# Kernel optimization log

Measured on AMD Instinct MI355X. Metric: run time of the kernel, lower is better.

## Reference

```python
import jax, jax.numpy as jnp
import numpy as np

N_NODES = 100000
N_EDGES = 400000
N_GRAPHS = 1000
DIM = 5
N_OUT = 2
EPS = 1e-5


def _linear_params(key, fan_in, fan_out):
    kw, kb = jax.random.split(key)
    s = 1.0 / np.sqrt(fan_in)
    w = jax.random.uniform(kw, (fan_in, fan_out), minval=-s, maxval=s, dtype=jnp.float32)
    b = jax.random.uniform(kb, (fan_out,), minval=-s, maxval=s, dtype=jnp.float32)
    return w, b


def _gn_params(c):
    # rows: [weight, bias, mean_scale] as in PyG GraphNorm init (1, 0, 1)
    return jnp.stack([jnp.ones((c,)), jnp.zeros((c,)), jnp.ones((c,))], axis=0).astype(jnp.float32)


def setup_inputs() -> dict:
    key = jax.random.key(0)
    ks = jax.random.split(key, 16)
    x = jax.random.normal(ks[0], (N_NODES, DIM), dtype=jnp.float32)
    edge_index = jax.random.randint(ks[1], (2, N_EDGES), 0, N_NODES, dtype=jnp.int64)
    batch = jnp.sort(jax.random.randint(ks[2], (N_NODES,), 0, N_GRAPHS, dtype=jnp.int64))
    c1_w1, c1_b1 = _linear_params(ks[3], 2 * DIM, 128)
    c1_w2, c1_b2 = _linear_params(ks[4], 128, 128)
    c1_w3, c1_b3 = _linear_params(ks[5], 128, 128)
    c2_w1, c2_b1 = _linear_params(ks[6], 2 * 128, 256)
    c2_w2, c2_b2 = _linear_params(ks[7], 256, 256)
    c3_w1, c3_b1 = _linear_params(ks[8], 2 * 256, 256)
    lin_w1, lin_b1 = _linear_params(ks[9], 256, 256)
    lin_w2, lin_b2 = _linear_params(ks[10], 256, N_OUT)
    return {
        "x": x, "edge_index": edge_index, "batch": batch,
        "c1_w1": c1_w1, "c1_b1": c1_b1, "c1_gn1": _gn_params(128),
        "c1_w2": c1_w2, "c1_b2": c1_b2, "c1_gn2": _gn_params(128),
        "c1_w3": c1_w3, "c1_b3": c1_b3, "c1_gn3": _gn_params(128),
        "c2_w1": c2_w1, "c2_b1": c2_b1, "c2_gn1": _gn_params(256),
        "c2_w2": c2_w2, "c2_b2": c2_b2, "c2_gn2": _gn_params(256),
        "c3_w1": c3_w1, "c3_b1": c3_b1, "c3_gn1": _gn_params(256),
        "lin_w1": lin_w1, "lin_b1": lin_b1, "lin_w2": lin_w2, "lin_b2": lin_b2,
    }


def _graph_norm(h, p):
    # PyG GraphNorm with batch=None: normalize over all rows (single graph)
    g, b, ms = p[0], p[1], p[2]
    m = h.mean(axis=0)
    out = h - ms * m
    var = (out * out).mean(axis=0)
    return g * out * jax.lax.rsqrt(var + EPS) + b


def _edge_conv(x, src, dst, layers):
    # EdgeConv message: nn(cat[x_i, x_j - x_i]) aggregated (mean) at target i
    xi = x[dst]                                     # [E, C]
    h = jnp.concatenate([xi, x[src] - xi], axis=-1)  # [E, 2C]
    for w, b, gp in layers:
        h = jax.nn.relu(_graph_norm(h @ w + b, gp))
    s = jax.ops.segment_sum(h, dst, num_segments=N_NODES)
    ones = jnp.ones((dst.shape[0], 1), dtype=h.dtype)
    cnt = jax.ops.segment_sum(ones, dst, num_segments=N_NODES)
    return s / jnp.maximum(cnt, 1.0)


def reference(x, edge_index, batch,
              c1_w1, c1_b1, c1_gn1, c1_w2, c1_b2, c1_gn2, c1_w3, c1_b3, c1_gn3,
              c2_w1, c2_b1, c2_gn1, c2_w2, c2_b2, c2_gn2,
              c3_w1, c3_b1, c3_gn1,
              lin_w1, lin_b1, lin_w2, lin_b2):
    src, dst = edge_index[0], edge_index[1]
    h = _edge_conv(x, src, dst, [(c1_w1, c1_b1, c1_gn1), (c1_w2, c1_b2, c1_gn2), (c1_w3, c1_b3, c1_gn3)])
    h = _edge_conv(h, src, dst, [(c2_w1, c2_b1, c2_gn1), (c2_w2, c2_b2, c2_gn2)])
    h = _edge_conv(h, src, dst, [(c3_w1, c3_b1, c3_gn1)])
    # global_mean_pool over graphs (dropout = identity in eval)
    gs = jax.ops.segment_sum(h, batch, num_segments=N_GRAPHS)
    gc = jax.ops.segment_sum(jnp.ones((h.shape[0], 1), h.dtype), batch, num_segments=N_GRAPHS)
    g = gs / jnp.maximum(gc, 1.0)                   # [G, 256]
    out = jax.nn.relu(g @ lin_w1 + lin_b1) @ lin_w2 + lin_b2  # [G, n_out]
    return out
```

## Files before the change

### kernel.cpp

```cpp
#include <hip/hip_runtime.h>
#include <hip/hip_bf16.h>

#define NN 100000
#define NE 400000
#define NG 1000

typedef __attribute__((ext_vector_type(8))) short bf16x8;
typedef __attribute__((ext_vector_type(4))) float f32x4;

__device__ __forceinline__ float bf2f(unsigned short h) {
    return __uint_as_float((unsigned)h << 16);
}
__device__ __forceinline__ unsigned short f2bf(float f) {
    unsigned u = __float_as_uint(f);
    return (unsigned short)((u + 0x7FFFu + ((u >> 16) & 1u)) >> 16);
}

__global__ void diag_kernel(float* __restrict__ out, int n, float val) {
    int i = blockIdx.x * 256 + threadIdx.x;
    if (i < n) out[i] = val;
}

__global__ void deg_kernel(const int* __restrict__ dst, int* __restrict__ deg) {
    int e = blockIdx.x * 256 + threadIdx.x;
    if (e < NE) atomicAdd(&deg[dst[e]], 1);
}

__global__ void invdeg_kernel(const int* __restrict__ deg, float* __restrict__ invdeg) {
    int n = blockIdx.x * 256 + threadIdx.x;
    if (n < NN) invdeg[n] = 1.0f / (float)(deg[n] > 0 ? deg[n] : 1);
}

__global__ void conv1_node_kernel(const float* __restrict__ x, const float* __restrict__ W,
                                  unsigned short* __restrict__ RQ) {
    __shared__ float Ws[1280];
    for (int i = threadIdx.x; i < 1280; i += 256) Ws[i] = W[i];
    __syncthreads();
    int c = threadIdx.x & 127;
    int which = threadIdx.x >> 7;
    for (int n = blockIdx.x; n < NN; n += gridDim.x) {
        float acc = 0.f;
        #pragma unroll
        for (int r = 0; r < 5; r++) {
            float xv = x[n * 5 + r];
            float bot = Ws[(5 + r) * 128 + c];
            float w = which ? bot : (Ws[r * 128 + c] - bot);
            acc = fmaf(xv, w, acc);
        }
        RQ[(size_t)n * 256 + threadIdx.x] = f2bf(acc);
    }
}

__global__ void wtrans_kernel(const float* __restrict__ W, unsigned short* __restrict__ Wt,
                              int K, int N) {
    int idx = blockIdx.x * 256 + threadIdx.x;
    if (idx >= K * N) return;
    int c = idx / K, k = idx - c * K;
    Wt[(size_t)c * K + k] = f2bf(W[(size_t)k * N + c]);
}

__global__ void wprime_t_kernel(const float* __restrict__ W, unsigned short* __restrict__ Wpt,
                                int K, int C) {
    int idx = blockIdx.x * 256 + threadIdx.x;
    if (idx >= 2 * C * K) return;
    int n = idx / K, k = idx - n * K;
    float v;
    if (n < C) v = W[(size_t)k * C + n] - W[(size_t)(K + k) * C + n];
    else       v = W[(size_t)(K + k) * C + (n - C)];
    Wpt[(size_t)n * K + k] = f2bf(v);
}

template<int C>
__global__ void gstats_kernel(const unsigned short* __restrict__ RQ, const int* __restrict__ src,
                              const int* __restrict__ dst, const float* __restrict__ bias,
                              float* __restrict__ ssum, float* __restrict__ ssq) {
    constexpr int EPB = 256 / C;
    int c = threadIdx.x % C;
    int sub = threadIdx.x / C;
    float b = bias[c];
    float ls = 0.f, lq = 0.f;
    for (int e = blockIdx.x * EPB + sub; e < NE; e += gridDim.x * EPB) {
        int d = dst[e], s = src[e];
        float v = (bf2f(RQ[(size_t)d * (2 * C) + c]) + bf2f(RQ[(size_t)s * (2 * C) + C + c])) + b;
        ls += v; lq += v * v;
    }
    __shared__ float red[2][256];
    red[0][threadIdx.x] = ls; red[1][threadIdx.x] = lq;
    __syncthreads();
    if (threadIdx.x < C) {
        float s0 = 0.f, q0 = 0.f;
        #pragma unroll
        for (int g = 0; g < EPB; g++) { s0 += red[0][g * C + c]; q0 += red[1][g * C + c]; }
        atomicAdd(&ssum[c], s0);
        atomicAdd(&ssq[c], q0);
    }
}

__global__ void finalize_kernel(const float* __restrict__ ssum, const float* __restrict__ ssq,
                                const float* __restrict__ gn, int C, float invM,
                                float* __restrict__ alpha, float* __restrict__ beta) {
    int c = threadIdx.x;
    if (c >= C) return;
    float g = gn[c], b = gn[C + c], ms = gn[2 * C + c];
    float m = ssum[c] * invM;
    float var = ssq[c] * invM - m * m * ms * (2.f - ms);
    float inv = rsqrtf(var + 1e-5f);
    alpha[c] = g * inv;
    beta[c] = b - g * inv * ms * m;
}

template<int BN, bool GATHER, bool NORMRELU, bool ROWSC, bool STATS, bool STORE, bool SCAT,
         bool AF32>
__global__ __launch_bounds__(256) void mgemm_kernel(
    const void* __restrict__ Av, const int* __restrict__ gsrc, const int* __restrict__ gdst,
    const float* __restrict__ biasIn, const unsigned short* __restrict__ Wt,
    const float* __restrict__ alpha, const float* __restrict__ beta,
    const float* __restrict__ rowscale, const float* __restrict__ biasOut,
    unsigned short* __restrict__ Cmat, int M, int K, int N,
    float* __restrict__ ssum, float* __restrict__ ssq,
    const float* __restrict__ alphaO, const float* __restrict__ betaO,
    float* __restrict__ hsum) {
    constexpr int WNC = BN / 4;
    constexpr int NF = WNC / 16;
    __shared__ __align__(16) unsigned short At[64][40];
    __shared__ __align__(16) unsigned short Bt[BN][40];
    __shared__ float sS[BN], sQ[BN];
    const int t = threadIdx.x;
    const int wave = t >> 6, lane = t & 63;
    const int l15 = lane & 15, lq = lane >> 4;
    const int r0 = blockIdx.y * 64;
    const int n0 = blockIdx.x * BN;
    const int srow = t >> 2, skq = t & 3;

    if (STATS && t < BN) { sS[t] = 0.f; sQ[t] = 0.f; }

    const int ar = r0 + srow;
    int gd = 0, gs = 0;
    if (GATHER) { gd = gdst[ar]; gs = gsrc[ar]; }
    float rs = 1.f;
    if (ROWSC) rs = (ar < M) ? rowscale[ar] : 0.f;

    const unsigned short* Abf = (const unsigned short*)Av;
    const float* Af = (const float*)Av;

    f32x4 acc[4][NF];
    #pragma unroll
    for (int i = 0; i < 4; i++)
        #pragma unroll
        for (int j = 0; j < NF; j++) acc[i][j] = {0.f, 0.f, 0.f, 0.f};

    for (int k0 = 0; k0 < K; k0 += 32) {
        const int kb = k0 + skq * 8;
        float v[8];
        if (GATHER) {
            ushort4 p0 = *(const ushort4*)&Abf[(size_t)gd * 2 * K + kb];
            ushort4 p1 = *(const ushort4*)&Abf[(size_t)gd * 2 * K + kb + 4];
            ushort4 q0 = *(const ushort4*)&Abf[(size_t)gs * 2 * K + K + kb];
            ushort4 q1 = *(const ushort4*)&Abf[(size_t)gs * 2 * K + K + kb + 4];
            float4 b0 = *(const float4*)&biasIn[kb];
            float4 b1 = *(const float4*)&biasIn[kb + 4];
            v[0] = bf2f(p0.x) + bf2f(q0.x) + b0.x; v[1] = bf2f(p0.y) + bf2f(q0.y) + b0.y;
            v[2] = bf2f(p0.z) + bf2f(q0.z) + b0.z; v[3] = bf2f(p0.w) + bf2f(q0.w) + b0.w;
            v[4] = bf2f(p1.x) + bf2f(q1.x) + b1.x; v[5] = bf2f(p1.y) + bf2f(q1.y) + b1.y;
            v[6] = bf2f(p1.z) + bf2f(q1.z) + b1.z; v[7] = bf2f(p1.w) + bf2f(q1.w) + b1.w;
        } else if (AF32) {
            if (ar < M) {
                float4 f0 = *(const float4*)&Af[(size_t)ar * K + kb];
                float4 f1 = *(const float4*)&Af[(size_t)ar * K + kb + 4];
                v[0] = f0.x; v[1] = f0.y; v[2] = f0.z; v[3] = f0.w;
                v[4] = f1.x; v[5] = f1.y; v[6] = f1.z; v[7] = f1.w;
            } else {
                #pragma unroll
                for (int i = 0; i < 8; i++) v[i] = 0.f;
            }
        } else {
            if (ar < M) {
                ushort4 p0 = *(const ushort4*)&Abf[(size_t)ar * K + kb];
                ushort4 p1 = *(const ushort4*)&Abf[(size_t)ar * K + kb + 4];
                v[0] = bf2f(p0.x); v[1] = bf2f(p0.y); v[2] = bf2f(p0.z); v[3] = bf2f(p0.w);
                v[4] = bf2f(p1.x); v[5] = bf2f(p1.y); v[6] = bf2f(p1.z); v[7] = bf2f(p1.w);
            } else {
                #pragma unroll
                for (int i = 0; i < 8; i++) v[i] = 0.f;
            }
        }
        if (NORMRELU) {
            float4 a0 = *(const float4*)&alpha[kb];
            float4 a1 = *(const float4*)&alpha[kb + 4];
            float4 e0 = *(const float4*)&beta[kb];
            float4 e1 = *(const float4*)&beta[kb + 4];
            float al[8] = {a0.x, a0.y, a0.z, a0.w, a1.x, a1.y, a1.z, a1.w};
            float be[8] = {e0.x, e0.y, e0.z, e0.w, e1.x, e1.y, e1.z, e1.w};
            #pragma unroll
            for (int i = 0; i < 8; i++) v[i] = fmaxf(fmaf(al[i], v[i], be[i]), 0.f);
        }
        if (ROWSC) {
            #pragma unroll
            for (int i = 0; i < 8; i++) v[i] *= rs;
        }
        uint pk[4];
        #pragma unroll
        for (int i = 0; i < 4; i++)
            pk[i] = (uint)f2bf(v[2 * i]) | ((uint)f2bf(v[2 * i + 1]) << 16);
        *(uint4*)&At[srow][skq * 8] = make_uint4(pk[0], pk[1], pk[2], pk[3]);

        for (int i = t; i < BN * 4; i += 256) {
            int col = i >> 2, kq = i & 3;
            *(uint4*)&Bt[col][kq * 8] =
                *(const uint4*)&Wt[(size_t)(n0 + col) * K + k0 + kq * 8];
        }
        __syncthreads();
        bf16x8 af[4];
        #pragma unroll
        for (int rf = 0; rf < 4; rf++)
            af[rf] = *(const bf16x8*)&At[16 * rf + l15][lq * 8];
        bf16x8 bfr[NF];
        #pragma unroll
        for (int cf = 0; cf < NF; cf++)
            bfr[cf] = *(const bf16x8*)&Bt[wave * WNC + 16 * cf + l15][lq * 8];
        #pragma unroll
        for (int rf = 0; rf < 4; rf++)
            #pragma unroll
            for (int cf = 0; cf < NF; cf++)
                acc[rf][cf] = __builtin_amdgcn_mfma_f32_16x16x32_bf16(
                    af[rf], bfr[cf], acc[rf][cf], 0, 0, 0);
        __syncthreads();
    }

    int cA[NF];
    float bO[NF], aO[NF], bOo[NF];
    #pragma unroll
    for (int cf = 0; cf < NF; cf++) {
        cA[cf] = n0 + wave * WNC + 16 * cf + l15;
        bO[cf] = (biasOut != nullptr) ? biasOut[cA[cf]] : 0.f;
        if (SCAT) { aO[cf] = alphaO[cA[cf]]; bOo[cf] = betaO[cA[cf]]; }
    }
    float ps[NF], pq[NF];
    #pragma unroll
    for (int cf = 0; cf < NF; cf++) { ps[cf] = 0.f; pq[cf] = 0.f; }
    #pragma unroll
    for (int rf = 0; rf < 4; rf++) {
        int rb = r0 + 16 * rf + lq * 4;
        int dd[4];
        if (SCAT) {
            #pragma unroll
            for (int jj = 0; jj < 4; jj++) dd[jj] = gdst[rb + jj];
        }
        #pragma unroll
        for (int cf = 0; cf < NF; cf++) {
            #pragma unroll
            for (int jj = 0; jj < 4; jj++) {
                float o = acc[rf][cf][jj] + bO[cf];
                if (STATS) { ps[cf] += o; pq[cf] += o * o; }
                if (STORE) {
                    int r = rb + jj;
                    if (r < M) Cmat[(size_t)r * N + cA[cf]] = f2bf(o);
                }
                if (SCAT) {
                    float h = fmaxf(fmaf(aO[cf], o, bOo[cf]), 0.f);
                    atomicAdd(&hsum[(size_t)dd[jj] * N + cA[cf]], h);
                }
            }
        }
    }
    if (STATS) {
        #pragma unroll
        for (int cf = 0; cf < NF; cf++) {
            float s = ps[cf], q = pq[cf];
            s += __shfl_xor(s, 16); s += __shfl_xor(s, 32);
            q += __shfl_xor(q, 16); q += __shfl_xor(q, 32);
            if (lq == 0) {
                atomicAdd(&sS[cA[cf] - n0], s);
                atomicAdd(&sQ[cA[cf] - n0], q);
            }
        }
        __syncthreads();
        if (t < BN) {
            atomicAdd(&ssum[n0 + t], sS[t]);
            atomicAdd(&ssq[n0 + t], sQ[t]);
        }
    }
}

template<int C>
__global__ void aggregate_kernel(const unsigned short* __restrict__ Y, const int* __restrict__ dst,
                                 const float* __restrict__ alpha, const float* __restrict__ beta,
                                 float* __restrict__ hsum) {
    constexpr int EPB = 256 / C;
    int c = threadIdx.x % C;
    int sub = threadIdx.x / C;
    float al = alpha[c], be = beta[c];
    for (int e = blockIdx.x * EPB + sub; e < NE; e += gridDim.x * EPB) {
        float v = fmaxf(fmaf(al, bf2f(Y[(size_t)e * C + c]), be), 0.f);
        atomicAdd(&hsum[(size_t)dst[e] * C + c], v);
    }
}

__global__ void aggregate_fg_kernel(const unsigned short* __restrict__ RQ,
                                    const int* __restrict__ src, const int* __restrict__ dst,
                                    const float* __restrict__ bias, const float* __restrict__ alpha,
                                    const float* __restrict__ beta, float* __restrict__ hsum) {
    int c = threadIdx.x;
    float b = bias[c], al = alpha[c], be = beta[c];
    for (int e = blockIdx.x; e < NE; e += gridDim.x) {
        int d = dst[e], s = src[e];
        float v = (bf2f(RQ[(size_t)d * 512 + c]) + bf2f(RQ[(size_t)s * 512 + 256 + c])) + b;
        float h = fmaxf(fmaf(al, v, be), 0.f);
        atomicAdd(&hsum[(size_t)d * 256 + c], h);
    }
}

__global__ void pool_kernel(const float* __restrict__ h3sum, const float* __restrict__ invdeg,
                            const int* __restrict__ batch, float* __restrict__ gsum,
                            int* __restrict__ gcnt) {
    int c = threadIdx.x;
    for (int n = blockIdx.x; n < NN; n += gridDim.x) {
        float v = h3sum[(size_t)n * 256 + c] * invdeg[n];
        int g = batch[n];
        atomicAdd(&gsum[(size_t)g * 256 + c], v);
        if (c == 0) atomicAdd(&gcnt[g], 1);
    }
}

__global__ void mlp_kernel(const float* __restrict__ gsum, const int* __restrict__ gcnt,
                           const float* __restrict__ W1, const float* __restrict__ b1,
                           const float* __restrict__ W2, const float* __restrict__ b2,
                           float* __restrict__ out) {
    int g = blockIdx.x;
    int t = threadIdx.x;
    __shared__ float grow[256];
    __shared__ float r0s[256], r1s[256];
    int cnt = gcnt[g];
    float inv = 1.0f / (float)(cnt > 0 ? cnt : 1);
    grow[t] = gsum[(size_t)g * 256 + t] * inv;
    __syncthreads();
    float acc = b1[t];
    for (int k = 0; k < 256; k++) acc = fmaf(grow[k], W1[k * 256 + t], acc);
    float h = fmaxf(acc, 0.f);
    r0s[t] = h * W2[t * 2 + 0];
    r1s[t] = h * W2[t * 2 + 1];
    __syncthreads();
    for (int s = 128; s > 0; s >>= 1) {
        if (t < s) { r0s[t] += r0s[t + s]; r1s[t] += r1s[t + s]; }
        __syncthreads();
    }
    if (t == 0) {
        out[g * 2 + 0] = r0s[0] + b2[0];
        out[g * 2 + 1] = r1s[0] + b2[1];
    }
}

extern "C" void kernel_launch(void* const* d_in, const int* in_sizes, int n_in,
                              void* d_out, int out_size, void* d_ws, size_t ws_size,
                              hipStream_t stream) {
    const float* x      = (const float*)d_in[0];
    const int*   ei     = (const int*)d_in[1];
    const int*   src    = ei;
    const int*   dstp   = ei + NE;
    const int*   batch  = (const int*)d_in[2];
    const float* c1_w1  = (const float*)d_in[3];
    const float* c1_b1  = (const float*)d_in[4];
    const float* c1_gn1 = (const float*)d_in[5];
    const float* c1_w2  = (const float*)d_in[6];
    const float* c1_b2  = (const float*)d_in[7];
    const float* c1_gn2 = (const float*)d_in[8];
    const float* c1_w3  = (const float*)d_in[9];
    const float* c1_b3  = (const float*)d_in[10];
    const float* c1_gn3 = (const float*)d_in[11];
    const float* c2_w1  = (const float*)d_in[12];
    const float* c2_b1  = (const float*)d_in[13];
    const float* c2_gn1 = (const float*)d_in[14];
    const float* c2_w2  = (const float*)d_in[15];
    const float* c2_b2  = (const float*)d_in[16];
    const float* c2_gn2 = (const float*)d_in[17];
    const float* c3_w1  = (const float*)d_in[18];
    const float* c3_b1  = (const float*)d_in[19];
    const float* c3_gn1 = (const float*)d_in[20];
    const float* lin_w1 = (const float*)d_in[21];
    const float* lin_b1 = (const float*)d_in[22];
    const float* lin_w2 = (const float*)d_in[23];
    const float* lin_b2 = (const float*)d_in[24];
    float* out = (float*)d_out;

    constexpr size_t REG_BYTES = (size_t)NE * 128 * 2;
    constexpr size_t NEED = 2 * REG_BYTES + 4 * 1024 * 1024;

    if (ws_size < NEED) {
        diag_kernel<<<(out_size + 255) / 256, 256, 0, stream>>>(
            out, out_size, (float)(ws_size >> 20));
        return;
    }

    char* base = (char*)d_ws;
    unsigned short* RA = (unsigned short*)base;
    unsigned short* RB = (unsigned short*)(base + REG_BYTES);
    float* h1sum = (float*)RB;
    float* h2sum = (float*)RB;
    float* h3sum = (float*)RB;
    char* p = base + 2 * REG_BYTES;
    auto alloc = [&](size_t bytes) -> void* {
        void* r = (void*)p;
        p += (bytes + 255) & ~(size_t)255;
        return r;
    };
    unsigned short* c1w2t = (unsigned short*)alloc((size_t)128 * 128 * 2);
    unsigned short* c1w3t = (unsigned short*)alloc((size_t)128 * 128 * 2);
    unsigned short* c2w2t = (unsigned short*)alloc((size_t)256 * 256 * 2);
    unsigned short* Wpt   = (unsigned short*)alloc((size_t)512 * 256 * 2);
    int*   deg    = (int*)alloc((size_t)NN * 4);
    float* invdeg = (float*)alloc((size_t)NN * 4);
    float* ssum   = (float*)alloc(256 * 4);
    float* ssq    = (float*)alloc(256 * 4);
    float* al0    = (float*)alloc(256 * 4);
    float* be0    = (float*)alloc(256 * 4);
    float* al1    = (float*)alloc(256 * 4);
    float* be1    = (float*)alloc(256 * 4);
    float* gsum   = (float*)alloc((size_t)NG * 256 * 4);
    int*   gcnt   = (int*)alloc((size_t)NG * 4);

    const float invE = 1.0f / (float)NE;
    const int MT_E = NE / 64;
    const int MT_N = (NN + 63) / 64;

    hipMemsetAsync(deg, 0, (size_t)NN * 4, stream);
    hipMemsetAsync(gsum, 0, (size_t)NG * 256 * 4, stream);
    hipMemsetAsync(gcnt, 0, (size_t)NG * 4, stream);

    deg_kernel<<<(NE + 255) / 256, 256, 0, stream>>>(dstp, deg);
    invdeg_kernel<<<(NN + 255) / 256, 256, 0, stream>>>(deg, invdeg);

    wtrans_kernel<<<(128 * 128 + 255) / 256, 256, 0, stream>>>(c1_w2, c1w2t, 128, 128);
    wtrans_kernel<<<(128 * 128 + 255) / 256, 256, 0, stream>>>(c1_w3, c1w3t, 128, 128);
    wtrans_kernel<<<(256 * 256 + 255) / 256, 256, 0, stream>>>(c2_w2, c2w2t, 256, 256);

    conv1_node_kernel<<<2048, 256, 0, stream>>>(x, c1_w1, RA);
    hipMemsetAsync(ssum, 0, 256 * 4, stream);
    hipMemsetAsync(ssq, 0, 256 * 4, stream);
    gstats_kernel<128><<<2048, 256, 0, stream>>>(RA, src, dstp, c1_b1, ssum, ssq);
    finalize_kernel<<<1, 256, 0, stream>>>(ssum, ssq, c1_gn1, 128, invE, al0, be0);

    hipMemsetAsync(ssum, 0, 256 * 4, stream);
    hipMemsetAsync(ssq, 0, 256 * 4, stream);
    mgemm_kernel<128, true, true, false, true, true, false, false>
        <<<dim3(1, MT_E), 256, 0, stream>>>(RA, src, dstp, c1_b1, c1w2t, al0, be0,
                                            nullptr, c1_b2, RB, NE, 128, 128,
                                            ssum, ssq, nullptr, nullptr, nullptr);
    finalize_kernel<<<1, 256, 0, stream>>>(ssum, ssq, c1_gn2, 128, invE, al0, be0);

    hipMemsetAsync(ssum, 0, 256 * 4, stream);
    hipMemsetAsync(ssq, 0, 256 * 4, stream);
    mgemm_kernel<128, false, true, false, true, true, false, false>
        <<<dim3(1, MT_E), 256, 0, stream>>>(RB, nullptr, nullptr, nullptr, c1w3t, al0, be0,
                                            nullptr, c1_b3, RA, NE, 128, 128,
                                            ssum, ssq, nullptr, nullptr, nullptr);
    finalize_kernel<<<1, 256, 0, stream>>>(ssum, ssq, c1_gn3, 128, invE, al0, be0);

    hipMemsetAsync(h1sum, 0, (size_t)NN * 128 * 4, stream);
    aggregate_kernel<128><<<2048, 256, 0, stream>>>(RA, dstp, al0, be0, h1sum);

    wprime_t_kernel<<<(512 * 128 + 255) / 256, 256, 0, stream>>>(c2_w1, Wpt, 128, 256);
    mgemm_kernel<256, false, false, true, false, true, false, true>
        <<<dim3(2, MT_N), 256, 0, stream>>>(h1sum, nullptr, nullptr, nullptr, Wpt,
                                            nullptr, nullptr, invdeg, nullptr, RA,
                                            NN, 128, 512, nullptr, nullptr,
                                            nullptr, nullptr, nullptr);
    hipMemsetAsync(ssum, 0, 256 * 4, stream);
    hipMemsetAsync(ssq, 0, 256 * 4, stream);
    gstats_kernel<256><<<2048, 256, 0, stream>>>(RA, src, dstp, c2_b1, ssum, ssq);
    finalize_kernel<<<1, 256, 0, stream>>>(ssum, ssq, c2_gn1, 256, invE, al0, be0);

    hipMemsetAsync(ssum, 0, 256 * 4, stream);
    hipMemsetAsync(ssq, 0, 256 * 4, stream);
    mgemm_kernel<256, true, true, false, true, false, false, false>
        <<<dim3(1, MT_E), 256, 0, stream>>>(RA, src, dstp, c2_b1, c2w2t, al0, be0,
                                            nullptr, c2_b2, nullptr, NE, 256, 256,
                                            ssum, ssq, nullptr, nullptr, nullptr);
    finalize_kernel<<<1, 256, 0, stream>>>(ssum, ssq, c2_gn2, 256, invE, al1, be1);

    hipMemsetAsync(h2sum, 0, (size_t)NN * 256 * 4, stream);
    mgemm_kernel<256, true, true, false, false, false, true, false>
        <<<dim3(1, MT_E), 256, 0, stream>>>(RA, src, dstp, c2_b1, c2w2t, al0, be0,
                                            nullptr, c2_b2, nullptr, NE, 256, 256,
                                            nullptr, nullptr, al1, be1, h2sum);

    wprime_t_kernel<<<(512 * 256 + 255) / 256, 256, 0, stream>>>(c3_w1, Wpt, 256, 256);
    mgemm_kernel<256, false, false, true, false, true, false, true>
        <<<dim3(2, MT_N), 256, 0, stream>>>(h2sum, nullptr, nullptr, nullptr, Wpt,
                                            nullptr, nullptr, invdeg, nullptr, RA,
                                            NN, 256, 512, nullptr, nullptr,
                                            nullptr, nullptr, nullptr);
    hipMemsetAsync(ssum, 0, 256 * 4, stream);
    hipMemsetAsync(ssq, 0, 256 * 4, stream);
    gstats_kernel<256><<<2048, 256, 0, stream>>>(RA, src, dstp, c3_b1, ssum, ssq);
    finalize_kernel<<<1, 256, 0, stream>>>(ssum, ssq, c3_gn1, 256, invE, al0, be0);

    hipMemsetAsync(h3sum, 0, (size_t)NN * 256 * 4, stream);
    aggregate_fg_kernel<<<2048, 256, 0, stream>>>(RA, src, dstp, c3_b1, al0, be0, h3sum);

    pool_kernel<<<2048, 256, 0, stream>>>(h3sum, invdeg, batch, gsum, gcnt);
    mlp_kernel<<<NG, 256, 0, stream>>>(gsum, gcnt, lin_w1, lin_b1, lin_w2, lin_b2, out);
}
```

Baseline: 2.477 ms.

## Vectorize edge kernels, register-prefetch GEMM B tiles, segment pooling accumulation

Edge-wise stats and aggregation kernels now have each thread handle 8 channels with 16-byte bf16 loads instead of scalar per-channel loads. The GEMM drops the shared B tile and reads weight fragments straight from global memory into registers, prefetching the next k-step, and double-buffers the A tile so there is one barrier per iteration. It also caches alpha, beta and bias in shared memory. Pooling exploits the sorted batch vector to accumulate runs of nodes locally before issuing one atomic per graph segment. These changes cut memory transactions and atomic contention, at the cost of more register pressure and scattered global reads for B.

After: 5.974 ms. 141% more time.

```diff
diff --git a/kernel.cpp b/kernel.cpp
--- a/kernel.cpp
+++ b/kernel.cpp
@@ -14,6 +14,20 @@
 __device__ __forceinline__ unsigned short f2bf(float f) {
     unsigned u = __float_as_uint(f);
     return (unsigned short)((u + 0x7FFFu + ((u >> 16) & 1u)) >> 16);
+}
+__device__ __forceinline__ void up8(uint4 u, float v[8]) {
+    v[0] = bf2f((unsigned short)u.x); v[1] = bf2f((unsigned short)(u.x >> 16));
+    v[2] = bf2f((unsigned short)u.y); v[3] = bf2f((unsigned short)(u.y >> 16));
+    v[4] = bf2f((unsigned short)u.z); v[5] = bf2f((unsigned short)(u.z >> 16));
+    v[6] = bf2f((unsigned short)u.w); v[7] = bf2f((unsigned short)(u.w >> 16));
+}
+__device__ __forceinline__ uint4 pk8(const float v[8]) {
+    uint4 r;
+    r.x = (uint)f2bf(v[0]) | ((uint)f2bf(v[1]) << 16);
+    r.y = (uint)f2bf(v[2]) | ((uint)f2bf(v[3]) << 16);
+    r.z = (uint)f2bf(v[4]) | ((uint)f2bf(v[5]) << 16);
+    r.w = (uint)f2bf(v[6]) | ((uint)f2bf(v[7]) << 16);
+    return r;
 }
 
 __global__ void diag_kernel(float* __restrict__ out, int n, float val) {
@@ -74,25 +88,43 @@
 __global__ void gstats_kernel(const unsigned short* __restrict__ RQ, const int* __restrict__ src,
                               const int* __restrict__ dst, const float* __restrict__ bias,
                               float* __restrict__ ssum, float* __restrict__ ssq) {
-    constexpr int EPB = 256 / C;
-    int c = threadIdx.x % C;
-    int sub = threadIdx.x / C;
-    float b = bias[c];
-    float ls = 0.f, lq = 0.f;
+    constexpr int LPE = C / 8;
+    constexpr int EPB = 256 / LPE;
+    const int t = threadIdx.x;
+    const int le = t % LPE, sub = t / LPE;
+    const int c0 = le * 8;
+    float4 b0 = *(const float4*)&bias[c0];
+    float4 b1 = *(const float4*)&bias[c0 + 4];
+    float bb[8] = {b0.x, b0.y, b0.z, b0.w, b1.x, b1.y, b1.z, b1.w};
+    float ls[8], lq[8];
+    #pragma unroll
+    for (int i = 0; i < 8; i++) { ls[i] = 0.f; lq[i] = 0.f; }
     for (int e = blockIdx.x * EPB + sub; e < NE; e += gridDim.x * EPB) {
         int d = dst[e], s = src[e];
-        float v = (bf2f(RQ[(size_t)d * (2 * C) + c]) + bf2f(RQ[(size_t)s * (2 * C) + C + c])) + b;
-        ls += v; lq += v * v;
-    }
-    __shared__ float red[2][256];
-    red[0][threadIdx.x] = ls; red[1][threadIdx.x] = lq;
+        uint4 rr = *(const uint4*)&RQ[(size_t)d * (2 * C) + c0];
+        uint4 qq = *(const uint4*)&RQ[(size_t)s * (2 * C) + C + c0];
+        float pr[8], pq[8];
+        up8(rr, pr); up8(qq, pq);
+        #pragma unroll
+        for (int i = 0; i < 8; i++) {
+            float v = pr[i] + pq[i] + bb[i];
+            ls[i] += v; lq[i] += v * v;
+        }
+    }
+    __shared__ float red[2][256][8];
+    #pragma unroll
+    for (int i = 0; i < 8; i++) { red[0][t][i] = ls[i]; red[1][t][i] = lq[i]; }
     __syncthreads();
-    if (threadIdx.x < C) {
-        float s0 = 0.f, q0 = 0.f;
-        #pragma unroll
-        for (int g = 0; g < EPB; g++) { s0 += red[0][g * C + c]; q0 += red[1][g * C + c]; }
-        atomicAdd(&ssum[c], s0);
-        atomicAdd(&ssq[c], q0);
+    if (t < C) {
+        int le2 = t >> 3, ch = t & 7;
+        float s = 0.f, q = 0.f;
+        #pragma unroll
+        for (int g = 0; g < EPB; g++) {
+            s += red[0][g * LPE + le2][ch];
+            q += red[1][g * LPE + le2][ch];
+        }
+        atomicAdd(&ssum[t], s);
+        atomicAdd(&ssq[t], q);
     }
 }
 
@@ -122,8 +154,8 @@
     float* __restrict__ hsum) {
     constexpr int WNC = BN / 4;
     constexpr int NF = WNC / 16;
-    __shared__ __align__(16) unsigned short At[64][40];
-    __shared__ __align__(16) unsigned short Bt[BN][40];
+    __shared__ __align__(16) unsigned short At[2][64][40];
+    __shared__ __align__(16) float sAl[256], sBe[256], sBi[256];
     __shared__ float sS[BN], sQ[BN];
     const int t = threadIdx.x;
     const int wave = t >> 6, lane = t & 63;
@@ -132,6 +164,8 @@
     const int n0 = blockIdx.x * BN;
     const int srow = t >> 2, skq = t & 3;
 
+    if (NORMRELU) for (int i = t; i < K; i += 256) { sAl[i] = alpha[i]; sBe[i] = beta[i]; }
+    if (GATHER)   for (int i = t; i < K; i += 256) { sBi[i] = biasIn[i]; }
     if (STATS && t < BN) { sS[t] = 0.f; sQ[t] = 0.f; }
 
     const int ar = r0 + srow;
@@ -143,52 +177,56 @@
     const unsigned short* Abf = (const unsigned short*)Av;
     const float* Af = (const float*)Av;
 
+    const unsigned short* bp[NF];
+    #pragma unroll
+    for (int cf = 0; cf < NF; cf++)
+        bp[cf] = &Wt[(size_t)(n0 + wave * WNC + 16 * cf + l15) * K + lq * 8];
+
     f32x4 acc[4][NF];
     #pragma unroll
     for (int i = 0; i < 4; i++)
         #pragma unroll
         for (int j = 0; j < NF; j++) acc[i][j] = {0.f, 0.f, 0.f, 0.f};
 
-    for (int k0 = 0; k0 < K; k0 += 32) {
-        const int kb = k0 + skq * 8;
+    uint4 rA, rQ;
+    float4 fA0, fA1;
+    auto loadRaw = [&](int k0, uint4& a, uint4& q, float4& f0, float4& f1) {
+        int kb = k0 + skq * 8;
+        if (GATHER) {
+            a = *(const uint4*)&Abf[(size_t)gd * (2 * K) + kb];
+            q = *(const uint4*)&Abf[(size_t)gs * (2 * K) + K + kb];
+        } else if (AF32) {
+            if (ar < M) {
+                f0 = *(const float4*)&Af[(size_t)ar * K + kb];
+                f1 = *(const float4*)&Af[(size_t)ar * K + kb + 4];
+            } else { f0 = make_float4(0, 0, 0, 0); f1 = f0; }
+        } else {
+            if (ar < M) a = *(const uint4*)&Abf[(size_t)ar * K + kb];
+            else a = make_uint4(0, 0, 0, 0);
+        }
+    };
+    auto stage = [&](int k0, int buf, uint4 a, uint4 q, float4 f0, float4 f1) {
+        int kb = k0 + skq * 8;
         float v[8];
         if (GATHER) {
-            ushort4 p0 = *(const ushort4*)&Abf[(size_t)gd * 2 * K + kb];
-            ushort4 p1 = *(const ushort4*)&Abf[(size_t)gd * 2 * K + kb + 4];
-            ushort4 q0 = *(const ushort4*)&Abf[(size_t)gs * 2 * K + K + kb];
-            ushort4 q1 = *(const ushort4*)&Abf[(size_t)gs * 2 * K + K + kb + 4];
-            float4 b0 = *(const float4*)&biasIn[kb];
-            float4 b1 = *(const float4*)&biasIn[kb + 4];
-            v[0] = bf2f(p0.x) + bf2f(q0.x) + b0.x; v[1] = bf2f(p0.y) + bf2f(q0.y) + b0.y;
-            v[2] = bf2f(p0.z) + bf2f(q0.z) + b0.z; v[3] = bf2f(p0.w) + bf2f(q0.w) + b0.w;
-            v[4] = bf2f(p1.x) + bf2f(q1.x) + b1.x; v[5] = bf2f(p1.y) + bf2f(q1.y) + b1.y;
-            v[6] = bf2f(p1.z) + bf2f(q1.z) + b1.z; v[7] = bf2f(p1.w) + bf2f(q1.w) + b1.w;
+            float pa[8], pq[8];
+            up8(a, pa); up8(q, pq);
+            float4 b0 = *(const float4*)&sBi[kb];
+            float4 b1 = *(const float4*)&sBi[kb + 4];
+            float bb[8] = {b0.x, b0.y, b0.z, b0.w, b1.x, b1.y, b1.z, b1.w};
+            #pragma unroll
+            for (int i = 0; i < 8; i++) v[i] = pa[i] + pq[i] + bb[i];
         } else if (AF32) {
-            if (ar < M) {
-                float4 f0 = *(const float4*)&Af[(size_t)ar * K + kb];
-                float4 f1 = *(const float4*)&Af[(size_t)ar * K + kb + 4];
-                v[0] = f0.x; v[1] = f0.y; v[2] = f0.z; v[3] = f0.w;
-                v[4] = f1.x; v[5] = f1.y; v[6] = f1.z; v[7] = f1.w;
-            } else {
-                #pragma unroll
-                for (int i = 0; i < 8; i++) v[i] = 0.f;
-            }
+            v[0] = f0.x; v[1] = f0.y; v[2] = f0.z; v[3] = f0.w;
+            v[4] = f1.x; v[5] = f1.y; v[6] = f1.z; v[7] = f1.w;
         } else {
-            if (ar < M) {
-                ushort4 p0 = *(const ushort4*)&Abf[(size_t)ar * K + kb];
-                ushort4 p1 = *(const ushort4*)&Abf[(size_t)ar * K + kb + 4];
-                v[0] = bf2f(p0.x); v[1] = bf2f(p0.y); v[2] = bf2f(p0.z); v[3] = bf2f(p0.w);
-                v[4] = bf2f(p1.x); v[5] = bf2f(p1.y); v[6] = bf2f(p1.z); v[7] = bf2f(p1.w);
-            } else {
-                #pragma unroll
-                for (int i = 0; i < 8; i++) v[i] = 0.f;
-            }
+            up8(a, v);
         }
         if (NORMRELU) {
-            float4 a0 = *(const float4*)&alpha[kb];
-            float4 a1 = *(const float4*)&alpha[kb + 4];
-            float4 e0 = *(const float4*)&beta[kb];
-            float4 e1 = *(const float4*)&beta[kb + 4];
+            float4 a0 = *(const float4*)&sAl[kb];
+            float4 a1 = *(const float4*)&sAl[kb + 4];
+            float4 e0 = *(const float4*)&sBe[kb];
+            float4 e1 = *(const float4*)&sBe[kb + 4];
             float al[8] = {a0.x, a0.y, a0.z, a0.w, a1.x, a1.y, a1.z, a1.w};
             float be[8] = {e0.x, e0.y, e0.z, e0.w, e1.x, e1.y, e1.z, e1.w};
             #pragma unroll
@@ -198,33 +236,45 @@
             #pragma unroll
             for (int i = 0; i < 8; i++) v[i] *= rs;
         }
-        uint pk[4];
-        #pragma unroll
-        for (int i = 0; i < 4; i++)
-            pk[i] = (uint)f2bf(v[2 * i]) | ((uint)f2bf(v[2 * i + 1]) << 16);
-        *(uint4*)&At[srow][skq * 8] = make_uint4(pk[0], pk[1], pk[2], pk[3]);
-
-        for (int i = t; i < BN * 4; i += 256) {
-            int col = i >> 2, kq = i & 3;
-            *(uint4*)&Bt[col][kq * 8] =
-                *(const uint4*)&Wt[(size_t)(n0 + col) * K + k0 + kq * 8];
-        }
-        __syncthreads();
+        *(uint4*)&At[buf][srow][skq * 8] = pk8(v);
+    };
+
+    loadRaw(0, rA, rQ, fA0, fA1);
+    bf16x8 bcur[NF];
+    #pragma unroll
+    for (int cf = 0; cf < NF; cf++) bcur[cf] = *(const bf16x8*)(bp[cf] + 0);
+    __syncthreads();
+    stage(0, 0, rA, rQ, fA0, fA1);
+    __syncthreads();
+
+    int buf = 0;
+    for (int k0 = 0; k0 < K; k0 += 32) {
+        int nxt = k0 + 32;
+        uint4 nA, nQ;
+        float4 nf0, nf1;
+        bf16x8 bnxt[NF];
+        if (nxt < K) {
+            loadRaw(nxt, nA, nQ, nf0, nf1);
+            #pragma unroll
+            for (int cf = 0; cf < NF; cf++) bnxt[cf] = *(const bf16x8*)(bp[cf] + nxt);
+        }
         bf16x8 af[4];
         #pragma unroll
         for (int rf = 0; rf < 4; rf++)
-            af[rf] = *(const bf16x8*)&At[16 * rf + l15][lq * 8];
-        bf16x8 bfr[NF];
-        #pragma unroll
-        for (int cf = 0; cf < NF; cf++)
-            bfr[cf] = *(const bf16x8*)&Bt[wave * WNC + 16 * cf + l15][lq * 8];
+            af[rf] = *(const bf16x8*)&At[buf][16 * rf + l15][lq * 8];
         #pragma unroll
         for (int rf = 0; rf < 4; rf++)
             #pragma unroll
             for (int cf = 0; cf < NF; cf++)
                 acc[rf][cf] = __builtin_amdgcn_mfma_f32_16x16x32_bf16(
-                    af[rf], bfr[cf], acc[rf][cf], 0, 0, 0);
-        __syncthreads();
+                    af[rf], bcur[cf], acc[rf][cf], 0, 0, 0);
+        if (nxt < K) {
+            stage(nxt, buf ^ 1, nA, nQ, nf0, nf1);
+            __syncthreads();
+            buf ^= 1;
+            #pragma unroll
+            for (int cf = 0; cf < NF; cf++) bcur[cf] = bnxt[cf];
+        }
     }
 
     int cA[NF];
@@ -286,13 +336,27 @@
 __global__ void aggregate_kernel(const unsigned short* __restrict__ Y, const int* __restrict__ dst,
                                  const float* __restrict__ alpha, const float* __restrict__ beta,
                                  float* __restrict__ hsum) {
-    constexpr int EPB = 256 / C;
-    int c = threadIdx.x % C;
-    int sub = threadIdx.x / C;
-    float al = alpha[c], be = beta[c];
+    constexpr int LPE = C / 8;
+    constexpr int EPB = 256 / LPE;
+    const int t = threadIdx.x;
+    const int le = t % LPE, sub = t / LPE;
+    const int c0 = le * 8;
+    float4 a0 = *(const float4*)&alpha[c0];
+    float4 a1 = *(const float4*)&alpha[c0 + 4];
+    float4 e0 = *(const float4*)&beta[c0];
+    float4 e1 = *(const float4*)&beta[c0 + 4];
+    float al[8] = {a0.x, a0.y, a0.z, a0.w, a1.x, a1.y, a1.z, a1.w};
+    float be[8] = {e0.x, e0.y, e0.z, e0.w, e1.x, e1.y, e1.z, e1.w};
     for (int e = blockIdx.x * EPB + sub; e < NE; e += gridDim.x * EPB) {
-        float v = fmaxf(fmaf(al, bf2f(Y[(size_t)e * C + c]), be), 0.f);
-        atomicAdd(&hsum[(size_t)dst[e] * C + c], v);
+        int d = dst[e];
+        uint4 yy = *(const uint4*)&Y[(size_t)e * C + c0];
+        float v[8];
+        up8(yy, v);
+        #pragma unroll
+        for (int i = 0; i < 8; i++) {
+            float h = fmaxf(fmaf(al[i], v[i], be[i]), 0.f);
+            atomicAdd(&hsum[(size_t)d * C + c0 + i], h);
+        }
     }
 }
 
@@ -300,26 +364,55 @@
                                     const int* __restrict__ src, const int* __restrict__ dst,
                                     const float* __restrict__ bias, const float* __restrict__ alpha,
                                     const float* __restrict__ beta, float* __restrict__ hsum) {
-    int c = threadIdx.x;
-    float b = bias[c], al = alpha[c], be = beta[c];
-    for (int e = blockIdx.x; e < NE; e += gridDim.x) {
+    const int t = threadIdx.x;
+    const int le = t & 31, sub = t >> 5;
+    const int c0 = le * 8;
+    float4 a0 = *(const float4*)&alpha[c0];
+    float4 a1 = *(const float4*)&alpha[c0 + 4];
+    float4 e0 = *(const float4*)&beta[c0];
+    float4 e1 = *(const float4*)&beta[c0 + 4];
+    float4 b0 = *(const float4*)&bias[c0];
+    float4 b1 = *(const float4*)&bias[c0 + 4];
+    float al[8] = {a0.x, a0.y, a0.z, a0.w, a1.x, a1.y, a1.z, a1.w};
+    float be[8] = {e0.x, e0.y, e0.z, e0.w, e1.x, e1.y, e1.z, e1.w};
+    float bb[8] = {b0.x, b0.y, b0.z, b0.w, b1.x, b1.y, b1.z, b1.w};
+    for (int e = blockIdx.x * 8 + sub; e < NE; e += gridDim.x * 8) {
         int d = dst[e], s = src[e];
-        float v = (bf2f(RQ[(size_t)d * 512 + c]) + bf2f(RQ[(size_t)s * 512 + 256 + c])) + b;
-        float h = fmaxf(fmaf(al, v, be), 0.f);
-        atomicAdd(&hsum[(size_t)d * 256 + c], h);
+        uint4 rr = *(const uint4*)&RQ[(size_t)d * 512 + c0];
+        uint4 qq = *(const uint4*)&RQ[(size_t)s * 512 + 256 + c0];
+        float pr[8], pq[8];
+        up8(rr, pr); up8(qq, pq);
+        #pragma unroll
+        for (int i = 0; i < 8; i++) {
+            float h = fmaxf(fmaf(al[i], pr[i] + pq[i] + bb[i], be[i]), 0.f);
+            atomicAdd(&hsum[(size_t)d * 256 + c0 + i], h);
+        }
     }
 }
 
 __global__ void pool_kernel(const float* __restrict__ h3sum, const float* __restrict__ invdeg,
                             const int* __restrict__ batch, float* __restrict__ gsum,
                             int* __restrict__ gcnt) {
-    int c = threadIdx.x;
-    for (int n = blockIdx.x; n < NN; n += gridDim.x) {
-        float v = h3sum[(size_t)n * 256 + c] * invdeg[n];
+    int chunk = (NN + gridDim.x - 1) / gridDim.x;
+    int nbeg = blockIdx.x * chunk;
+    int nend = min(nbeg + chunk, NN);
+    if (nbeg >= nend) return;
+    int t = threadIdx.x;
+    int curg = batch[nbeg];
+    float acc = 0.f;
+    int cnt = 0;
+    for (int n = nbeg; n < nend; n++) {
         int g = batch[n];
-        atomicAdd(&gsum[(size_t)g * 256 + c], v);
-        if (c == 0) atomicAdd(&gcnt[g], 1);
-    }
+        if (g != curg) {
+            atomicAdd(&gsum[(size_t)curg * 256 + t], acc);
+            if (t == 0) atomicAdd(&gcnt[curg], cnt);
+            curg = g; acc = 0.f; cnt = 0;
+        }
+        acc += h3sum[(size_t)n * 256 + t] * invdeg[n];
+        cnt++;
+    }
+    atomicAdd(&gsum[(size_t)curg * 256 + t], acc);
+    if (t == 0) atomicAdd(&gcnt[curg], cnt);
 }
 
 __global__ void mlp_kernel(const float* __restrict__ gsum, const int* __restrict__ gcnt,
@@ -497,6 +590,6 @@
     hipMemsetAsync(h3sum, 0, (size_t)NN * 256 * 4, stream);
     aggregate_fg_kernel<<<2048, 256, 0, stream>>>(RA, src, dstp, c3_b1, al0, be0, h3sum);
 
-    pool_kernel<<<2048, 256, 0, stream>>>(h3sum, invdeg, batch, gsum, gcnt);
+    pool_kernel<<<512, 256, 0, stream>>>(h3sum, invdeg, batch, gsum, gcnt);
     mlp_kernel<<<NG, 256, 0, stream>>>(gsum, gcnt, lin_w1, lin_b1, lin_w2, lin_b2, out);
 }
```
